# Performance work log

Hardware: AMD Instinct MI355X
Metric: run time of the kernel (lower is better)

## Reference

```python
import math
import jax, jax.numpy as jnp
import numpy as np

B, LQ, LK, D, DV = 16, 2048, 2048, 256, 256


def setup_inputs() -> dict:
    key = jax.random.key(0)
    k1, k2, k3, k4 = jax.random.split(key, 4)
    query = jax.random.normal(k1, (B, LQ, D), dtype=jnp.float32)
    kmat = jax.random.normal(k2, (B, LK, D), dtype=jnp.float32)
    value = jax.random.normal(k3, (B, LK, DV), dtype=jnp.float32)
    # per-batch valid lengths in [1, LK] (avoid 0 => all -inf row)
    valid_len = jax.random.randint(k4, (B,), 1, LK + 1, dtype=jnp.int64)
    return {"query": query, "key": kmat, "value": value, "valid_len": valid_len}


def reference(query, key, value, valid_len):
    d = query.shape[-1]
    # [B, Lq, Lk] scaled dot-product scores
    scores = jnp.einsum("bqd,bkd->bqk", query, key) / math.sqrt(d)
    # mask positions k >= valid_len[b] (same mask broadcast over all queries,
    # matching the repeat(1, Lq).view(shape) in the original masked_softmax)
    mask = jnp.arange(key.shape[1])[None, None, :] < valid_len[:, None, None]
    scores = jnp.where(mask, scores, -jnp.inf)
    attn = jax.nn.softmax(scores, axis=-1)  # dropout rate is 0.0 => identity
    return jnp.einsum("bqk,bkv->bqv", attn, value)
```

## Files before the change

kernel.cpp:

```cpp
#include <hip/hip_runtime.h>
#include <hip/hip_bf16.h>

#define B_   16
#define LQ_  2048
#define LK_  2048
#define D_   256
#define DV_  256
#define MINF -1.0e30f

typedef __bf16 bf16x8_t __attribute__((ext_vector_type(8)));
typedef short  s16x8    __attribute__((ext_vector_type(8)));
typedef short  s16x4    __attribute__((ext_vector_type(4)));
typedef float  f32x4    __attribute__((ext_vector_type(4)));

__device__ __forceinline__ unsigned short f2bf(float f) {
  unsigned int u = __builtin_bit_cast(unsigned int, f);
  u += 0x7fffu + ((u >> 16) & 1u);
  return (unsigned short)(u >> 16);
}

__device__ __forceinline__ s16x8 pack8(float4 a, float4 b) {
  s16x8 r;
  r[0] = (short)f2bf(a.x); r[1] = (short)f2bf(a.y);
  r[2] = (short)f2bf(a.z); r[3] = (short)f2bf(a.w);
  r[4] = (short)f2bf(b.x); r[5] = (short)f2bf(b.y);
  r[6] = (short)f2bf(b.z); r[7] = (short)f2bf(b.w);
  return r;
}

__device__ __forceinline__ void glds16(const unsigned short* g, unsigned short* l) {
  __builtin_amdgcn_global_load_lds(
      (const __attribute__((address_space(1))) unsigned int*)g,
      (__attribute__((address_space(3))) unsigned int*)l, 16, 0, 0);
}

__global__ __launch_bounds__(256) void prep_k(const float* __restrict__ K,
                                              unsigned short* __restrict__ wsK) {
  int gid = blockIdx.x * 256 + threadIdx.x;
  int gr = gid >> 5;
  int c  = gid & 31;
  const float* src = K + ((size_t)gr << 8) + c * 8;
  float4 a = *(const float4*)(src);
  float4 b = *(const float4*)(src + 4);
  *(s16x8*)(wsK + ((size_t)gr << 8) + ((c ^ (gr & 7)) << 3)) = pack8(a, b);
}

__global__ __launch_bounds__(256) void prep_v(const float* __restrict__ V,
                                              unsigned short* __restrict__ wsV) {
  __shared__ unsigned short t[256 * 72];
  const int tid = threadIdx.x;
  const float* src = V + (size_t)blockIdx.x * 64 * 256;
  #pragma unroll
  for (int i = 0; i < 16; ++i) {
    int idx = i * 256 + tid;
    int k   = idx >> 6;
    int dv0 = (idx & 63) * 4;
    float4 x = *(const float4*)(src + k * 256 + dv0);
    t[(dv0 + 0) * 72 + k] = f2bf(x.x);
    t[(dv0 + 1) * 72 + k] = f2bf(x.y);
    t[(dv0 + 2) * 72 + k] = f2bf(x.z);
    t[(dv0 + 3) * 72 + k] = f2bf(x.w);
  }
  __syncthreads();
  unsigned short* dst = wsV + (size_t)blockIdx.x * 16384;
  #pragma unroll
  for (int i = 0; i < 8; ++i) {
    int idx = i * 256 + tid;
    int dv = idx >> 3;
    int ch = idx & 7;
    s16x8 v = *(const s16x8*)(&t[dv * 72 + ch * 8]);
    *(s16x8*)(dst + dv * 64 + ((ch ^ (dv & 7)) << 3)) = v;
  }
}

__global__ __launch_bounds__(512) void attn_fwd3(
    const float* __restrict__ Q, const unsigned short* __restrict__ wsK,
    const unsigned short* __restrict__ wsV, const int* __restrict__ VL,
    float* __restrict__ O) {
  __shared__ __align__(16) unsigned short lds_s[4][16384];

  const int tid  = threadIdx.x;
  const int wid  = tid >> 6;
  const int lane = tid & 63;
  const int l15  = lane & 15;
  const int lg   = lane >> 4;
  const int rg   = wid & 3;
  const int kh   = wid >> 2;

  const int bid = blockIdx.x;
  const int b   = bid >> 5;
  const int qt  = bid & 31;

  int n_k = (VL[1] == 0) ? VL[2 * b] : VL[b];
  if (n_k < 1) n_k = 1;
  if (n_k > LK_) n_k = LK_;
  const int nt = (n_k + 63) >> 6;

  const int qbase = qt * 64 + rg * 16;

  s16x8 qf[8];
  {
    const float* qp = Q + ((size_t)b * LQ_ + qbase + l15) * D_ + lg * 8;
    #pragma unroll
    for (int dk = 0; dk < 8; ++dk) {
      float4 a = *(const float4*)(qp + dk * 32);
      float4 c = *(const float4*)(qp + dk * 32 + 4);
      qf[dk] = pack8(a, c);
    }
  }

  f32x4 o[16];
  #pragma unroll
  for (int c = 0; c < 16; ++c) o[c] = (f32x4){0.f, 0.f, 0.f, 0.f};
  float m = MINF, l = 0.f;

  const unsigned short* kbw = wsK + (size_t)b * LK_ * D_;
  const unsigned short* vbw = wsV + (size_t)b * LK_ * DV_;

#define STAGE(buf, t) do {                                                   \
    const unsigned short* ks_ = kbw + (size_t)(t) * 16384;                   \
    const unsigned short* vs_ = vbw + (size_t)(t) * 16384;                   \
    _Pragma("unroll")                                                        \
    for (int p = 0; p < 4; ++p) {                                            \
      int cu = p * 512 + wid * 64;                                           \
      glds16(ks_ + (size_t)(cu + lane) * 8, &lds_s[(buf)][cu * 8]);          \
      glds16(vs_ + (size_t)(cu + lane) * 8, &lds_s[2 + (buf)][cu * 8]);      \
    }                                                                        \
  } while (0)

  STAGE(0, 0);
  __syncthreads();

  for (int t = 0; t < nt; ++t) {
    const int cur = t & 1;
    if (t + 1 < nt) STAGE(cur ^ 1, t + 1);

    const unsigned short* kl = &lds_s[cur][0];
    f32x4 s[2];
    __builtin_amdgcn_s_setprio(1);
    #pragma unroll
    for (int kc = 0; kc < 2; ++kc) {
      int krow = kh * 32 + kc * 16 + l15;
      int sw = (krow & 7) << 3;
      const unsigned short* base = kl + krow * 256;
      f32x4 a0 = (f32x4){0.f, 0.f, 0.f, 0.f};
      f32x4 a1 = (f32x4){0.f, 0.f, 0.f, 0.f};
      #pragma unroll
      for (int dk = 0; dk < 4; ++dk) {
        s16x8 k0 = *(const s16x8*)(base + ((dk * 64 + lg * 8) ^ sw));
        s16x8 k1 = *(const s16x8*)(base + ((dk * 64 + 32 + lg * 8) ^ sw));
        a0 = __builtin_amdgcn_mfma_f32_16x16x32_bf16(
            __builtin_bit_cast(bf16x8_t, k0),
            __builtin_bit_cast(bf16x8_t, qf[2 * dk]), a0, 0, 0, 0);
        a1 = __builtin_amdgcn_mfma_f32_16x16x32_bf16(
            __builtin_bit_cast(bf16x8_t, k1),
            __builtin_bit_cast(bf16x8_t, qf[2 * dk + 1]), a1, 0, 0, 0);
      }
      s[kc] = a0 + a1;
    }
    __builtin_amdgcn_s_setprio(0);

    #pragma unroll
    for (int kc = 0; kc < 2; ++kc) {
      int gk = t * 64 + kh * 32 + kc * 16 + lg * 4;
      #pragma unroll
      for (int j = 0; j < 4; ++j)
        s[kc][j] = (gk + j < n_k) ? s[kc][j] * 0.0625f : MINF;
    }

    float pm = s[0][0];
    pm = fmaxf(pm, s[0][1]); pm = fmaxf(pm, s[0][2]); pm = fmaxf(pm, s[0][3]);
    pm = fmaxf(pm, s[1][0]); pm = fmaxf(pm, s[1][1]);
    pm = fmaxf(pm, s[1][2]); pm = fmaxf(pm, s[1][3]);
    pm = fmaxf(pm, __shfl_xor(pm, 16, 64));
    pm = fmaxf(pm, __shfl_xor(pm, 32, 64));
    if (__any(pm > m + 8.0f)) {
      float mn = fmaxf(m, pm);
      float sc = __expf(m - mn);
      m = mn; l *= sc;
      #pragma unroll
      for (int c = 0; c < 16; ++c) o[c] = o[c] * sc;
    }
    float p0[4], p1[4];
    #pragma unroll
    for (int j = 0; j < 4; ++j) {
      p0[j] = __expf(s[0][j] - m);
      p1[j] = __expf(s[1][j] - m);
    }
    float ps = ((p0[0] + p0[1]) + (p0[2] + p0[3]))
             + ((p1[0] + p1[1]) + (p1[2] + p1[3]));
    ps += __shfl_xor(ps, 16, 64);
    ps += __shfl_xor(ps, 32, 64);
    l += ps;

    float pv8[8];
    int sl0 = l15 + ((lg & 1) ? 32 : 0);
    #pragma unroll
    for (int h = 0; h < 2; ++h) {
      int sl = sl0 + h * 16;
      #pragma unroll
      for (int j = 0; j < 4; ++j) {
        float a  = __shfl(p0[j], sl, 64);
        float bb = __shfl(p1[j], sl, 64);
        pv8[h * 4 + j] = (lg >= 2) ? bb : a;
      }
    }
    s16x8 pb;
    #pragma unroll
    for (int e = 0; e < 8; ++e) pb[e] = (short)f2bf(pv8[e]);

    const unsigned short* vl_ = &lds_s[2 + cur][0];
    __builtin_amdgcn_s_setprio(1);
    #pragma unroll
    for (int c = 0; c < 16; ++c) {
      int dv = c * 16 + l15;
      int off = dv * 64 + (((kh * 4 + lg) ^ (dv & 7)) << 3);
      s16x8 vf = *(const s16x8*)(vl_ + off);
      o[c] = __builtin_amdgcn_mfma_f32_16x16x32_bf16(
          __builtin_bit_cast(bf16x8_t, vf),
          __builtin_bit_cast(bf16x8_t, pb), o[c], 0, 0, 0);
    }
    __builtin_amdgcn_s_setprio(0);

    __syncthreads();
  }

  float* mrg = (float*)&lds_s[0][0];
  float* mo  = mrg + (wid & 3) * 4160;
  if (wid >= 4) {
    #pragma unroll
    for (int c = 0; c < 16; ++c)
      #pragma unroll
      for (int j = 0; j < 4; ++j)
        mo[l15 * 257 + c * 16 + lg * 4 + j] = o[c][j];
    mo[4112 + l15] = m;
    mo[4128 + l15] = l;
  }
  __syncthreads();
  if (wid < 4) {
    float mb = mo[4112 + l15];
    float lb = mo[4128 + l15];
    float M  = fmaxf(m, mb);
    float sa = __expf(m - M), sb = __expf(mb - M);
    float invL = 1.0f / (sa * l + sb * lb);
    float* ob = O + ((size_t)b * LQ_ + qbase + l15) * DV_;
    #pragma unroll
    for (int c = 0; c < 16; ++c) {
      int dvb = c * 16 + lg * 4;
      const float* mr = mo + l15 * 257 + dvb;
      float4 r;
      r.x = (sa * o[c][0] + sb * mr[0]) * invL;
      r.y = (sa * o[c][1] + sb * mr[1]) * invL;
      r.z = (sa * o[c][2] + sb * mr[2]) * invL;
      r.w = (sa * o[c][3] + sb * mr[3]) * invL;
      *(float4*)(ob + dvb) = r;
    }
  }
#undef STAGE
}

__global__ __launch_bounds__(256) void attn_fwd(
    const float* __restrict__ Q, const float* __restrict__ K,
    const float* __restrict__ V, const int* __restrict__ VL,
    float* __restrict__ O) {
  __shared__ __align__(16) unsigned short lds_k[64 * D_];
  __shared__ __align__(16) unsigned short lds_v[DV_ * 64];
  __shared__ __align__(16) unsigned short lds_p[4][16 * 64];

  const int tid  = threadIdx.x;
  const int wid  = tid >> 6;
  const int lane = tid & 63;
  const int l15  = lane & 15;
  const int lg   = lane >> 4;
  const int bid = blockIdx.x;
  const int b   = bid >> 5;
  const int qt  = bid & 31;

  int n_k = (VL[1] == 0) ? VL[2 * b] : VL[b];
  if (n_k < 1) n_k = 1;
  if (n_k > LK_) n_k = LK_;

  const int qbase = qt * 64 + wid * 16;
  s16x8 qf[8];
  {
    const float* qp = Q + ((size_t)b * LQ_ + qbase + l15) * D_ + lg * 8;
    #pragma unroll
    for (int dk = 0; dk < 8; ++dk) {
      float4 a = *(const float4*)(qp + dk * 32);
      float4 c = *(const float4*)(qp + dk * 32 + 4);
      qf[dk] = pack8(a, c);
    }
  }
  f32x4 o[16];
  #pragma unroll
  for (int c = 0; c < 16; ++c) o[c] = (f32x4){0.f, 0.f, 0.f, 0.f};
  float m[4]    = {-INFINITY, -INFINITY, -INFINITY, -INFINITY};
  float lsum[4] = {0.f, 0.f, 0.f, 0.f};
  const float* kb = K + (size_t)b * LK_ * D_;
  const float* vb = V + (size_t)b * LK_ * DV_;
  const int nt = (n_k + 63) / 64;

  for (int kt = 0; kt < nt; ++kt) {
    __syncthreads();
    {
      const float* src = kb + (size_t)kt * 64 * D_;
      #pragma unroll
      for (int p = 0; p < 8; ++p) {
        int e = (p * 256 + tid) * 8;
        int r = e >> 8;
        int d = e & 255;
        float4 a = *(const float4*)(src + e);
        float4 c = *(const float4*)(src + e + 4);
        *(s16x8*)(&lds_k[r * 256 + (d ^ ((r & 7) << 3))]) = pack8(a, c);
      }
    }
    {
      const float* src = vb + (size_t)kt * 64 * DV_;
      #pragma unroll
      for (int p = 0; p < 2; ++p) {
        int item = p * 256 + tid;
        int k0  = (item >> 5) * 4;
        int dv0 = (item & 31) * 8;
        float va[4][8];
        #pragma unroll
        for (int r = 0; r < 4; ++r) {
          float4 x = *(const float4*)(src + (k0 + r) * DV_ + dv0);
          float4 y = *(const float4*)(src + (k0 + r) * DV_ + dv0 + 4);
          va[r][0]=x.x; va[r][1]=x.y; va[r][2]=x.z; va[r][3]=x.w;
          va[r][4]=y.x; va[r][5]=y.y; va[r][6]=y.z; va[r][7]=y.w;
        }
        #pragma unroll
        for (int i = 0; i < 8; ++i) {
          int dv = dv0 + i;
          s16x4 w;
          w[0]=(short)f2bf(va[0][i]); w[1]=(short)f2bf(va[1][i]);
          w[2]=(short)f2bf(va[2][i]); w[3]=(short)f2bf(va[3][i]);
          *(s16x4*)(&lds_v[dv * 64 + (k0 ^ ((dv & 7) << 3))]) = w;
        }
      }
    }
    __syncthreads();

    f32x4 s[4];
    #pragma unroll
    for (int kc = 0; kc < 4; ++kc) {
      f32x4 acc = (f32x4){0.f, 0.f, 0.f, 0.f};
      int krow = kc * 16 + l15;
      int sw = (krow & 7) << 3;
      #pragma unroll
      for (int dk = 0; dk < 8; ++dk) {
        s16x8 kf = *(const s16x8*)(&lds_k[krow * 256 + ((dk * 32 + lg * 8) ^ sw)]);
        acc = __builtin_amdgcn_mfma_f32_16x16x32_bf16(
            __builtin_bit_cast(bf16x8_t, qf[dk]),
            __builtin_bit_cast(bf16x8_t, kf), acc, 0, 0, 0);
      }
      s[kc] = acc;
    }
    #pragma unroll
    for (int kc = 0; kc < 4; ++kc) {
      int gk = kt * 64 + kc * 16 + l15;
      #pragma unroll
      for (int j = 0; j < 4; ++j) {
        float v = s[kc][j] * 0.0625f;
        s[kc][j] = (gk < n_k) ? v : -INFINITY;
      }
    }
    float pm[4];
    #pragma unroll
    for (int j = 0; j < 4; ++j)
      pm[j] = fmaxf(fmaxf(s[0][j], s[1][j]), fmaxf(s[2][j], s[3][j]));
    #pragma unroll
    for (int off = 1; off < 16; off <<= 1) {
      #pragma unroll
      for (int j = 0; j < 4; ++j)
        pm[j] = fmaxf(pm[j], __shfl_xor(pm[j], off, 64));
    }
    float sc[4];
    #pragma unroll
    for (int j = 0; j < 4; ++j) {
      float mn = fmaxf(m[j], pm[j]);
      sc[j] = __expf(m[j] - mn);
      m[j] = mn;
    }
    float psum[4] = {0.f, 0.f, 0.f, 0.f};
    #pragma unroll
    for (int kc = 0; kc < 4; ++kc) {
      #pragma unroll
      for (int j = 0; j < 4; ++j) {
        float p = __expf(s[kc][j] - m[j]);
        psum[j] += p;
        int r = lg * 4 + j;
        lds_p[wid][r * 64 + ((kc * 16 + l15) ^ ((r & 7) << 3))] = f2bf(p);
      }
    }
    #pragma unroll
    for (int off = 1; off < 16; off <<= 1) {
      #pragma unroll
      for (int j = 0; j < 4; ++j)
        psum[j] += __shfl_xor(psum[j], off, 64);
    }
    #pragma unroll
    for (int j = 0; j < 4; ++j) lsum[j] = lsum[j] * sc[j] + psum[j];
    #pragma unroll
    for (int c = 0; c < 16; ++c) {
      #pragma unroll
      for (int j = 0; j < 4; ++j) o[c][j] *= sc[j];
    }
    s16x8 pa[2];
    #pragma unroll
    for (int kk = 0; kk < 2; ++kk)
      pa[kk] = *(const s16x8*)(&lds_p[wid][l15 * 64 + ((kk * 32 + lg * 8) ^ ((l15 & 7) << 3))]);
    #pragma unroll
    for (int c = 0; c < 16; ++c) {
      #pragma unroll
      for (int kk = 0; kk < 2; ++kk) {
        int dv = c * 16 + l15;
        s16x8 vf = *(const s16x8*)(&lds_v[dv * 64 + ((kk * 32 + lg * 8) ^ ((dv & 7) << 3))]);
        o[c] = __builtin_amdgcn_mfma_f32_16x16x32_bf16(
            __builtin_bit_cast(bf16x8_t, pa[kk]),
            __builtin_bit_cast(bf16x8_t, vf), o[c], 0, 0, 0);
      }
    }
  }
  float inv[4];
  #pragma unroll
  for (int j = 0; j < 4; ++j) inv[j] = 1.0f / lsum[j];
  float* ob = O + ((size_t)b * LQ_ + qbase) * DV_;
  #pragma unroll
  for (int c = 0; c < 16; ++c) {
    #pragma unroll
    for (int j = 0; j < 4; ++j) {
      int r = lg * 4 + j;
      ob[(size_t)r * DV_ + c * 16 + l15] = o[c][j] * inv[j];
    }
  }
}

extern "C" void kernel_launch(void* const* d_in, const int* in_sizes, int n_in,
                              void* d_out, int out_size, void* d_ws, size_t ws_size,
                              hipStream_t stream) {
  const float* Q  = (const float*)d_in[0];
  const float* K  = (const float*)d_in[1];
  const float* V  = (const float*)d_in[2];
  const int*   VL = (const int*)d_in[3];
  float* O = (float*)d_out;

  const size_t kv_elems = (size_t)B_ * LK_ * D_;
  const size_t need = kv_elems * 2 * sizeof(unsigned short);
  if (ws_size >= need) {
    unsigned short* wsK = (unsigned short*)d_ws;
    unsigned short* wsV = wsK + kv_elems;
    prep_k<<<dim3(4096), dim3(256), 0, stream>>>(K, wsK);
    prep_v<<<dim3(512), dim3(256), 0, stream>>>(V, wsV);
    attn_fwd3<<<dim3(512), dim3(512), 0, stream>>>(Q, wsK, wsV, VL, O);
  } else {
    attn_fwd<<<dim3(512), dim3(256), 0, stream>>>(Q, K, V, VL, O);
  }
}
```

Baseline: 135.7 us.

## Double query rows per wave to reuse K/V fragments across two MFMA tiles

Each wave now handles 32 query rows (two 16-row chunks) instead of 16, so every K and V fragment read from LDS feeds two MFMAs. The block covers 128 queries and the grid is halved to 256 blocks. The P-matrix shuffle is replaced by a per-wave LDS scratch round-trip. This reduces LDS traffic per FLOP and K/V staging per query, but doubles accumulator registers (launch_bounds 512,2) and halves grid parallelism, which on a 256-CU part could leave CUs underused.

```diff
diff --git a/kernel.cpp b/kernel.cpp
--- a/kernel.cpp
+++ b/kernel.cpp
@@ -73,59 +73,64 @@
   }
 }
 
-__global__ __launch_bounds__(512) void attn_fwd3(
+__global__ __launch_bounds__(512, 2) void attn_fwd4(
     const float* __restrict__ Q, const unsigned short* __restrict__ wsK,
     const unsigned short* __restrict__ wsV, const int* __restrict__ VL,
     float* __restrict__ O) {
-  __shared__ __align__(16) unsigned short lds_s[4][16384];
+  __shared__ __align__(16) unsigned short lds_all[75776];
 
   const int tid  = threadIdx.x;
   const int wid  = tid >> 6;
   const int lane = tid & 63;
   const int l15  = lane & 15;
   const int lg   = lane >> 4;
-  const int rg   = wid & 3;
+  const int rq   = wid & 3;
   const int kh   = wid >> 2;
 
   const int bid = blockIdx.x;
-  const int b   = bid >> 5;
-  const int qt  = bid & 31;
+  const int b   = bid >> 4;
+  const int qt  = bid & 15;
 
   int n_k = (VL[1] == 0) ? VL[2 * b] : VL[b];
   if (n_k < 1) n_k = 1;
   if (n_k > LK_) n_k = LK_;
   const int nt = (n_k + 63) >> 6;
 
-  const int qbase = qt * 64 + rg * 16;
-
-  s16x8 qf[8];
-  {
-    const float* qp = Q + ((size_t)b * LQ_ + qbase + l15) * D_ + lg * 8;
+  const int qbase = qt * 128 + rq * 32;
+
+  s16x8 qf[2][8];
+  #pragma unroll
+  for (int qc = 0; qc < 2; ++qc) {
+    const float* qp = Q + ((size_t)b * LQ_ + qbase + qc * 16 + l15) * D_ + lg * 8;
     #pragma unroll
     for (int dk = 0; dk < 8; ++dk) {
       float4 a = *(const float4*)(qp + dk * 32);
       float4 c = *(const float4*)(qp + dk * 32 + 4);
-      qf[dk] = pack8(a, c);
-    }
-  }
-
-  f32x4 o[16];
-  #pragma unroll
-  for (int c = 0; c < 16; ++c) o[c] = (f32x4){0.f, 0.f, 0.f, 0.f};
-  float m = MINF, l = 0.f;
+      qf[qc][dk] = pack8(a, c);
+    }
+  }
+
+  f32x4 o[2][16];
+  #pragma unroll
+  for (int qc = 0; qc < 2; ++qc)
+    #pragma unroll
+    for (int c = 0; c < 16; ++c) o[qc][c] = (f32x4){0.f, 0.f, 0.f, 0.f};
+  float m[2] = {MINF, MINF}, l[2] = {0.f, 0.f};
 
   const unsigned short* kbw = wsK + (size_t)b * LK_ * D_;
   const unsigned short* vbw = wsV + (size_t)b * LK_ * DV_;
-
-#define STAGE(buf, t) do {                                                   \
-    const unsigned short* ks_ = kbw + (size_t)(t) * 16384;                   \
-    const unsigned short* vs_ = vbw + (size_t)(t) * 16384;                   \
-    _Pragma("unroll")                                                        \
-    for (int p = 0; p < 4; ++p) {                                            \
-      int cu = p * 512 + wid * 64;                                           \
-      glds16(ks_ + (size_t)(cu + lane) * 8, &lds_s[(buf)][cu * 8]);          \
-      glds16(vs_ + (size_t)(cu + lane) * 8, &lds_s[2 + (buf)][cu * 8]);      \
-    }                                                                        \
+  unsigned short* pw = &lds_all[65536 + wid * 1280];
+
+#define STAGE(buf, t) do {                                                    \
+    const unsigned short* ks_ = kbw + (size_t)(t) * 16384;                    \
+    const unsigned short* vs_ = vbw + (size_t)(t) * 16384;                    \
+    _Pragma("unroll")                                                         \
+    for (int p = 0; p < 4; ++p) {                                             \
+      int cu = p * 512 + wid * 64;                                            \
+      glds16(ks_ + (size_t)(cu + lane) * 8, &lds_all[(buf) * 16384 + cu * 8]);\
+      glds16(vs_ + (size_t)(cu + lane) * 8,                                   \
+             &lds_all[32768 + (buf) * 16384 + cu * 8]);                       \
+    }                                                                         \
   } while (0)
 
   STAGE(0, 0);
@@ -135,8 +140,8 @@
     const int cur = t & 1;
     if (t + 1 < nt) STAGE(cur ^ 1, t + 1);
 
-    const unsigned short* kl = &lds_s[cur][0];
-    f32x4 s[2];
+    const unsigned short* kl = &lds_all[cur * 16384];
+    f32x4 s[2][2];
     __builtin_amdgcn_s_setprio(1);
     #pragma unroll
     for (int kc = 0; kc < 2; ++kc) {
@@ -146,17 +151,17 @@
       f32x4 a0 = (f32x4){0.f, 0.f, 0.f, 0.f};
       f32x4 a1 = (f32x4){0.f, 0.f, 0.f, 0.f};
       #pragma unroll
-      for (int dk = 0; dk < 4; ++dk) {
-        s16x8 k0 = *(const s16x8*)(base + ((dk * 64 + lg * 8) ^ sw));
-        s16x8 k1 = *(const s16x8*)(base + ((dk * 64 + 32 + lg * 8) ^ sw));
+      for (int dk = 0; dk < 8; ++dk) {
+        s16x8 kf = *(const s16x8*)(base + ((dk * 32 + lg * 8) ^ sw));
         a0 = __builtin_amdgcn_mfma_f32_16x16x32_bf16(
-            __builtin_bit_cast(bf16x8_t, k0),
-            __builtin_bit_cast(bf16x8_t, qf[2 * dk]), a0, 0, 0, 0);
+            __builtin_bit_cast(bf16x8_t, kf),
+            __builtin_bit_cast(bf16x8_t, qf[0][dk]), a0, 0, 0, 0);
         a1 = __builtin_amdgcn_mfma_f32_16x16x32_bf16(
-            __builtin_bit_cast(bf16x8_t, k1),
-            __builtin_bit_cast(bf16x8_t, qf[2 * dk + 1]), a1, 0, 0, 0);
-      }
-      s[kc] = a0 + a1;
+            __builtin_bit_cast(bf16x8_t, kf),
+            __builtin_bit_cast(bf16x8_t, qf[1][dk]), a1, 0, 0, 0);
+      }
+      s[kc][0] = a0;
+      s[kc][1] = a1;
     }
     __builtin_amdgcn_s_setprio(0);
 
@@ -164,96 +169,108 @@
     for (int kc = 0; kc < 2; ++kc) {
       int gk = t * 64 + kh * 32 + kc * 16 + lg * 4;
       #pragma unroll
-      for (int j = 0; j < 4; ++j)
-        s[kc][j] = (gk + j < n_k) ? s[kc][j] * 0.0625f : MINF;
-    }
-
-    float pm = s[0][0];
-    pm = fmaxf(pm, s[0][1]); pm = fmaxf(pm, s[0][2]); pm = fmaxf(pm, s[0][3]);
-    pm = fmaxf(pm, s[1][0]); pm = fmaxf(pm, s[1][1]);
-    pm = fmaxf(pm, s[1][2]); pm = fmaxf(pm, s[1][3]);
-    pm = fmaxf(pm, __shfl_xor(pm, 16, 64));
-    pm = fmaxf(pm, __shfl_xor(pm, 32, 64));
-    if (__any(pm > m + 8.0f)) {
-      float mn = fmaxf(m, pm);
-      float sc = __expf(m - mn);
-      m = mn; l *= sc;
-      #pragma unroll
-      for (int c = 0; c < 16; ++c) o[c] = o[c] * sc;
-    }
-    float p0[4], p1[4];
-    #pragma unroll
-    for (int j = 0; j < 4; ++j) {
-      p0[j] = __expf(s[0][j] - m);
-      p1[j] = __expf(s[1][j] - m);
-    }
-    float ps = ((p0[0] + p0[1]) + (p0[2] + p0[3]))
-             + ((p1[0] + p1[1]) + (p1[2] + p1[3]));
-    ps += __shfl_xor(ps, 16, 64);
-    ps += __shfl_xor(ps, 32, 64);
-    l += ps;
-
-    float pv8[8];
-    int sl0 = l15 + ((lg & 1) ? 32 : 0);
-    #pragma unroll
-    for (int h = 0; h < 2; ++h) {
-      int sl = sl0 + h * 16;
-      #pragma unroll
-      for (int j = 0; j < 4; ++j) {
-        float a  = __shfl(p0[j], sl, 64);
-        float bb = __shfl(p1[j], sl, 64);
-        pv8[h * 4 + j] = (lg >= 2) ? bb : a;
-      }
-    }
-    s16x8 pb;
-    #pragma unroll
-    for (int e = 0; e < 8; ++e) pb[e] = (short)f2bf(pv8[e]);
-
-    const unsigned short* vl_ = &lds_s[2 + cur][0];
+      for (int qc = 0; qc < 2; ++qc)
+        #pragma unroll
+        for (int j = 0; j < 4; ++j)
+          s[kc][qc][j] = (gk + j < n_k) ? s[kc][qc][j] * 0.0625f : MINF;
+    }
+
+    float pm[2];
+    #pragma unroll
+    for (int qc = 0; qc < 2; ++qc) {
+      float v = fmaxf(fmaxf(s[0][qc][0], s[0][qc][1]),
+                      fmaxf(s[0][qc][2], s[0][qc][3]));
+      v = fmaxf(v, fmaxf(fmaxf(s[1][qc][0], s[1][qc][1]),
+                         fmaxf(s[1][qc][2], s[1][qc][3])));
+      v = fmaxf(v, __shfl_xor(v, 16, 64));
+      v = fmaxf(v, __shfl_xor(v, 32, 64));
+      pm[qc] = v;
+    }
+    if (__any((pm[0] > m[0] + 8.0f) || (pm[1] > m[1] + 8.0f))) {
+      #pragma unroll
+      for (int qc = 0; qc < 2; ++qc) {
+        float mn = fmaxf(m[qc], pm[qc]);
+        float sc = __expf(m[qc] - mn);
+        m[qc] = mn; l[qc] *= sc;
+        #pragma unroll
+        for (int c = 0; c < 16; ++c) o[qc][c] = o[qc][c] * sc;
+      }
+    }
+    #pragma unroll
+    for (int qc = 0; qc < 2; ++qc) {
+      float p[2][4];
+      #pragma unroll
+      for (int kc = 0; kc < 2; ++kc)
+        #pragma unroll
+        for (int j = 0; j < 4; ++j)
+          p[kc][j] = __expf(s[kc][qc][j] - m[qc]);
+      float ps = ((p[0][0] + p[0][1]) + (p[0][2] + p[0][3]))
+               + ((p[1][0] + p[1][1]) + (p[1][2] + p[1][3]));
+      ps += __shfl_xor(ps, 16, 64);
+      ps += __shfl_xor(ps, 32, 64);
+      l[qc] += ps;
+      #pragma unroll
+      for (int kc = 0; kc < 2; ++kc) {
+        s16x4 w;
+        w[0] = (short)f2bf(p[kc][0]); w[1] = (short)f2bf(p[kc][1]);
+        w[2] = (short)f2bf(p[kc][2]); w[3] = (short)f2bf(p[kc][3]);
+        *(s16x4*)(pw + (qc * 16 + l15) * 40 + kc * 16 + lg * 4) = w;
+      }
+    }
+
+    s16x8 pb[2];
+    #pragma unroll
+    for (int qc = 0; qc < 2; ++qc)
+      pb[qc] = *(const s16x8*)(pw + (qc * 16 + l15) * 40 + lg * 8);
+
+    const unsigned short* vl_ = &lds_all[32768 + cur * 16384];
     __builtin_amdgcn_s_setprio(1);
     #pragma unroll
     for (int c = 0; c < 16; ++c) {
       int dv = c * 16 + l15;
-      int off = dv * 64 + (((kh * 4 + lg) ^ (dv & 7)) << 3);
-      s16x8 vf = *(const s16x8*)(vl_ + off);
-      o[c] = __builtin_amdgcn_mfma_f32_16x16x32_bf16(
+      s16x8 vf = *(const s16x8*)(vl_ + dv * 64 + (((kh * 4 + lg) ^ (dv & 7)) << 3));
+      o[0][c] = __builtin_amdgcn_mfma_f32_16x16x32_bf16(
           __builtin_bit_cast(bf16x8_t, vf),
-          __builtin_bit_cast(bf16x8_t, pb), o[c], 0, 0, 0);
+          __builtin_bit_cast(bf16x8_t, pb[0]), o[0][c], 0, 0, 0);
+      o[1][c] = __builtin_amdgcn_mfma_f32_16x16x32_bf16(
+          __builtin_bit_cast(bf16x8_t, vf),
+          __builtin_bit_cast(bf16x8_t, pb[1]), o[1][c], 0, 0, 0);
     }
     __builtin_amdgcn_s_setprio(0);
 
     __syncthreads();
   }
 
-  float* mrg = (float*)&lds_s[0][0];
-  float* mo  = mrg + (wid & 3) * 4160;
-  if (wid >= 4) {
-    #pragma unroll
-    for (int c = 0; c < 16; ++c)
-      #pragma unroll
-      for (int j = 0; j < 4; ++j)
-        mo[l15 * 257 + c * 16 + lg * 4 + j] = o[c][j];
-    mo[4112 + l15] = m;
-    mo[4128 + l15] = l;
+  float* mo = (float*)lds_all + rq * 8448;
+  if (kh == 1) {
+    #pragma unroll
+    for (int qc = 0; qc < 2; ++qc) {
+      #pragma unroll
+      for (int c = 0; c < 16; ++c)
+        *(f32x4*)(mo + (qc * 16 + l15) * 260 + c * 16 + lg * 4) = o[qc][c];
+      mo[8320 + qc * 16 + l15] = m[qc];
+      mo[8352 + qc * 16 + l15] = l[qc];
+    }
   }
   __syncthreads();
-  if (wid < 4) {
-    float mb = mo[4112 + l15];
-    float lb = mo[4128 + l15];
-    float M  = fmaxf(m, mb);
-    float sa = __expf(m - M), sb = __expf(mb - M);
-    float invL = 1.0f / (sa * l + sb * lb);
-    float* ob = O + ((size_t)b * LQ_ + qbase + l15) * DV_;
-    #pragma unroll
-    for (int c = 0; c < 16; ++c) {
-      int dvb = c * 16 + lg * 4;
-      const float* mr = mo + l15 * 257 + dvb;
-      float4 r;
-      r.x = (sa * o[c][0] + sb * mr[0]) * invL;
-      r.y = (sa * o[c][1] + sb * mr[1]) * invL;
-      r.z = (sa * o[c][2] + sb * mr[2]) * invL;
-      r.w = (sa * o[c][3] + sb * mr[3]) * invL;
-      *(float4*)(ob + dvb) = r;
+  if (kh == 0) {
+    #pragma unroll
+    for (int qc = 0; qc < 2; ++qc) {
+      float mb = mo[8320 + qc * 16 + l15];
+      float lb = mo[8352 + qc * 16 + l15];
+      float M  = fmaxf(m[qc], mb);
+      float sa = __expf(m[qc] - M), sb = __expf(mb - M);
+      float invL = 1.0f / (sa * l[qc] + sb * lb);
+      float* ob = O + ((size_t)b * LQ_ + qbase + qc * 16 + l15) * DV_;
+      #pragma unroll
+      for (int c = 0; c < 16; ++c) {
+        int dvb = c * 16 + lg * 4;
+        f32x4 mr = *(const f32x4*)(mo + (qc * 16 + l15) * 260 + dvb);
+        f32x4 r;
+        #pragma unroll
+        for (int j = 0; j < 4; ++j) r[j] = (sa * o[qc][c][j] + sb * mr[j]) * invL;
+        *(f32x4*)(ob + dvb) = r;
+      }
     }
   }
 #undef STAGE
@@ -452,7 +469,7 @@
     unsigned short* wsV = wsK + kv_elems;
     prep_k<<<dim3(4096), dim3(256), 0, stream>>>(K, wsK);
     prep_v<<<dim3(512), dim3(256), 0, stream>>>(V, wsV);
-    attn_fwd3<<<dim3(512), dim3(512), 0, stream>>>(Q, wsK, wsV, VL, O);
+    attn_fwd4<<<dim3(256), dim3(512), 0, stream>>>(Q, wsK, wsV, VL, O);
   } else {
     attn_fwd<<<dim3(512), dim3(256), 0, stream>>>(Q, K, V, VL, O);
   }
```

Result: no change. 135.9 us (+0.2%).

## Halve KV tile to 32 keys to cut LDS and raise occupancy

Applied to the files above, without the earlier changes.

The KV tile per iteration shrinks from 64 to 32 keys. That cuts the LDS footprint from 128KB to about 67KB and allows more blocks per CU, with launch bounds set to (512,4). The V transpose layout is rebuilt for 32-key tiles, and the PV product switches to a 16x16x16 bf16 MFMA, which removes the cross-lane shuffles that rearranged probabilities. It also adds manual vmcnt waits with raw barriers, and a block-index remap that interleaves batches across blocks. The trade-off is twice as many loop iterations and barriers, plus smaller, less efficient MFMAs.

```diff
diff --git a/kernel.cpp b/kernel.cpp
--- a/kernel.cpp
+++ b/kernel.cpp
@@ -32,6 +32,17 @@
   __builtin_amdgcn_global_load_lds(
       (const __attribute__((address_space(1))) unsigned int*)g,
       (__attribute__((address_space(3))) unsigned int*)l, 16, 0, 0);
+}
+
+__device__ __forceinline__ f32x4 mfma16(s16x4 a, s16x4 b, f32x4 c) {
+#if __has_builtin(__builtin_amdgcn_mfma_f32_16x16x16bf16_1k)
+  return __builtin_amdgcn_mfma_f32_16x16x16bf16_1k(a, b, c, 0, 0, 0);
+#else
+  f32x4 d;
+  asm volatile("v_mfma_f32_16x16x16_bf16 %0, %1, %2, %3"
+               : "=v"(d) : "v"(a), "v"(b), "v"(c));
+  return d;
+#endif
 }
 
 __global__ __launch_bounds__(256) void prep_k(const float* __restrict__ K,
@@ -47,56 +58,58 @@
 
 __global__ __launch_bounds__(256) void prep_v(const float* __restrict__ V,
                                               unsigned short* __restrict__ wsV) {
-  __shared__ unsigned short t[256 * 72];
+  __shared__ unsigned short t[256 * 40];
   const int tid = threadIdx.x;
-  const float* src = V + (size_t)blockIdx.x * 64 * 256;
-  #pragma unroll
-  for (int i = 0; i < 16; ++i) {
+  const float* src = V + (size_t)blockIdx.x * 32 * 256;
+  #pragma unroll
+  for (int i = 0; i < 8; ++i) {
     int idx = i * 256 + tid;
     int k   = idx >> 6;
     int dv0 = (idx & 63) * 4;
     float4 x = *(const float4*)(src + k * 256 + dv0);
-    t[(dv0 + 0) * 72 + k] = f2bf(x.x);
-    t[(dv0 + 1) * 72 + k] = f2bf(x.y);
-    t[(dv0 + 2) * 72 + k] = f2bf(x.z);
-    t[(dv0 + 3) * 72 + k] = f2bf(x.w);
+    t[(dv0 + 0) * 40 + k] = f2bf(x.x);
+    t[(dv0 + 1) * 40 + k] = f2bf(x.y);
+    t[(dv0 + 2) * 40 + k] = f2bf(x.z);
+    t[(dv0 + 3) * 40 + k] = f2bf(x.w);
   }
   __syncthreads();
-  unsigned short* dst = wsV + (size_t)blockIdx.x * 16384;
-  #pragma unroll
-  for (int i = 0; i < 8; ++i) {
+  unsigned short* dst = wsV + (size_t)blockIdx.x * 8192;
+  #pragma unroll
+  for (int i = 0; i < 4; ++i) {
     int idx = i * 256 + tid;
-    int dv = idx >> 3;
-    int ch = idx & 7;
-    s16x8 v = *(const s16x8*)(&t[dv * 72 + ch * 8]);
-    *(s16x8*)(dst + dv * 64 + ((ch ^ (dv & 7)) << 3)) = v;
-  }
-}
-
-__global__ __launch_bounds__(512) void attn_fwd3(
+    int dv = idx >> 2;
+    int cs = idx & 3;
+    int c2 = cs ^ ((dv >> 1) & 3);
+    s16x8 v = *(const s16x8*)(&t[dv * 40 + cs * 8]);
+    *(s16x8*)(dst + dv * 32 + c2 * 8) = v;
+  }
+}
+
+__global__ __launch_bounds__(512, 4) void attn_fwd8(
     const float* __restrict__ Q, const unsigned short* __restrict__ wsK,
     const unsigned short* __restrict__ wsV, const int* __restrict__ VL,
     float* __restrict__ O) {
-  __shared__ __align__(16) unsigned short lds_s[4][16384];
+  __shared__ __align__(16) unsigned short lds_all[33536];
 
   const int tid  = threadIdx.x;
   const int wid  = tid >> 6;
   const int lane = tid & 63;
   const int l15  = lane & 15;
   const int lg   = lane >> 4;
-  const int rg   = wid & 3;
+  const int rq   = wid & 3;
   const int kh   = wid >> 2;
 
   const int bid = blockIdx.x;
-  const int b   = bid >> 5;
-  const int qt  = bid & 31;
+  const int j   = bid >> 3;
+  const int b   = (bid & 7) + ((j >> 5) << 3);
+  const int qt  = j & 31;
 
   int n_k = (VL[1] == 0) ? VL[2 * b] : VL[b];
   if (n_k < 1) n_k = 1;
   if (n_k > LK_) n_k = LK_;
-  const int nt = (n_k + 63) >> 6;
-
-  const int qbase = qt * 64 + rg * 16;
+  const int nt = (n_k + 31) >> 5;
+
+  const int qbase = qt * 64 + rq * 16;
 
   s16x8 qf[8];
   {
@@ -117,61 +130,60 @@
   const unsigned short* kbw = wsK + (size_t)b * LK_ * D_;
   const unsigned short* vbw = wsV + (size_t)b * LK_ * DV_;
 
-#define STAGE(buf, t) do {                                                   \
-    const unsigned short* ks_ = kbw + (size_t)(t) * 16384;                   \
-    const unsigned short* vs_ = vbw + (size_t)(t) * 16384;                   \
-    _Pragma("unroll")                                                        \
-    for (int p = 0; p < 4; ++p) {                                            \
-      int cu = p * 512 + wid * 64;                                           \
-      glds16(ks_ + (size_t)(cu + lane) * 8, &lds_s[(buf)][cu * 8]);          \
-      glds16(vs_ + (size_t)(cu + lane) * 8, &lds_s[2 + (buf)][cu * 8]);      \
-    }                                                                        \
+#define STAGE(buf, t) do {                                                    \
+    const unsigned short* ks_ = kbw + (size_t)(t) * 8192;                     \
+    const unsigned short* vs_ = vbw + (size_t)(t) * 8192;                     \
+    _Pragma("unroll")                                                         \
+    for (int p = 0; p < 2; ++p) {                                             \
+      int cu = p * 512 + wid * 64;                                            \
+      glds16(ks_ + (size_t)(cu + lane) * 8, &lds_all[(buf) * 8192 + cu * 8]); \
+      glds16(vs_ + (size_t)(cu + lane) * 8,                                   \
+             &lds_all[16384 + (buf) * 8192 + cu * 8]);                        \
+    }                                                                         \
   } while (0)
 
   STAGE(0, 0);
-  __syncthreads();
 
   for (int t = 0; t < nt; ++t) {
     const int cur = t & 1;
-    if (t + 1 < nt) STAGE(cur ^ 1, t + 1);
-
-    const unsigned short* kl = &lds_s[cur][0];
-    f32x4 s[2];
+    if (t + 1 < nt) {
+      STAGE(cur ^ 1, t + 1);
+      asm volatile("s_waitcnt vmcnt(4)" ::: "memory");
+    } else {
+      asm volatile("s_waitcnt vmcnt(0)" ::: "memory");
+    }
+    __builtin_amdgcn_s_barrier();
+    __builtin_amdgcn_sched_barrier(0);
+
+    const unsigned short* kl = &lds_all[cur * 8192];
+    const int krow = kh * 16 + l15;
+    const int sw = (krow & 7) << 3;
+    const unsigned short* kbase = kl + krow * 256;
+    f32x4 a0 = (f32x4){0.f, 0.f, 0.f, 0.f};
+    f32x4 a1 = (f32x4){0.f, 0.f, 0.f, 0.f};
     __builtin_amdgcn_s_setprio(1);
     #pragma unroll
-    for (int kc = 0; kc < 2; ++kc) {
-      int krow = kh * 32 + kc * 16 + l15;
-      int sw = (krow & 7) << 3;
-      const unsigned short* base = kl + krow * 256;
-      f32x4 a0 = (f32x4){0.f, 0.f, 0.f, 0.f};
-      f32x4 a1 = (f32x4){0.f, 0.f, 0.f, 0.f};
-      #pragma unroll
-      for (int dk = 0; dk < 4; ++dk) {
-        s16x8 k0 = *(const s16x8*)(base + ((dk * 64 + lg * 8) ^ sw));
-        s16x8 k1 = *(const s16x8*)(base + ((dk * 64 + 32 + lg * 8) ^ sw));
-        a0 = __builtin_amdgcn_mfma_f32_16x16x32_bf16(
-            __builtin_bit_cast(bf16x8_t, k0),
-            __builtin_bit_cast(bf16x8_t, qf[2 * dk]), a0, 0, 0, 0);
-        a1 = __builtin_amdgcn_mfma_f32_16x16x32_bf16(
-            __builtin_bit_cast(bf16x8_t, k1),
-            __builtin_bit_cast(bf16x8_t, qf[2 * dk + 1]), a1, 0, 0, 0);
-      }
-      s[kc] = a0 + a1;
+    for (int dk = 0; dk < 4; ++dk) {
+      s16x8 k0 = *(const s16x8*)(kbase + ((dk * 64 + lg * 8) ^ sw));
+      s16x8 k1 = *(const s16x8*)(kbase + ((dk * 64 + 32 + lg * 8) ^ sw));
+      a0 = __builtin_amdgcn_mfma_f32_16x16x32_bf16(
+          __builtin_bit_cast(bf16x8_t, k0),
+          __builtin_bit_cast(bf16x8_t, qf[2 * dk]), a0, 0, 0, 0);
+      a1 = __builtin_amdgcn_mfma_f32_16x16x32_bf16(
+          __builtin_bit_cast(bf16x8_t, k1),
+          __builtin_bit_cast(bf16x8_t, qf[2 * dk + 1]), a1, 0, 0, 0);
     }
     __builtin_amdgcn_s_setprio(0);
-
-    #pragma unroll
-    for (int kc = 0; kc < 2; ++kc) {
-      int gk = t * 64 + kh * 32 + kc * 16 + lg * 4;
-      #pragma unroll
-      for (int j = 0; j < 4; ++j)
-        s[kc][j] = (gk + j < n_k) ? s[kc][j] * 0.0625f : MINF;
-    }
-
-    float pm = s[0][0];
-    pm = fmaxf(pm, s[0][1]); pm = fmaxf(pm, s[0][2]); pm = fmaxf(pm, s[0][3]);
-    pm = fmaxf(pm, s[1][0]); pm = fmaxf(pm, s[1][1]);
-    pm = fmaxf(pm, s[1][2]); pm = fmaxf(pm, s[1][3]);
+    f32x4 s = a0 + a1;
+
+    {
+      int gk = t * 32 + kh * 16 + lg * 4;
+      #pragma unroll
+      for (int j2 = 0; j2 < 4; ++j2)
+        s[j2] = (gk + j2 < n_k) ? s[j2] * 0.0625f : MINF;
+    }
+
+    float pm = fmaxf(fmaxf(s[0], s[1]), fmaxf(s[2], s[3]));
     pm = fmaxf(pm, __shfl_xor(pm, 16, 64));
     pm = fmaxf(pm, __shfl_xor(pm, 32, 64));
     if (__any(pm > m + 8.0f)) {
@@ -181,79 +193,59 @@
       #pragma unroll
       for (int c = 0; c < 16; ++c) o[c] = o[c] * sc;
     }
-    float p0[4], p1[4];
-    #pragma unroll
-    for (int j = 0; j < 4; ++j) {
-      p0[j] = __expf(s[0][j] - m);
-      p1[j] = __expf(s[1][j] - m);
-    }
-    float ps = ((p0[0] + p0[1]) + (p0[2] + p0[3]))
-             + ((p1[0] + p1[1]) + (p1[2] + p1[3]));
+    float p[4];
+    #pragma unroll
+    for (int j2 = 0; j2 < 4; ++j2) p[j2] = __expf(s[j2] - m);
+    float ps = (p[0] + p[1]) + (p[2] + p[3]);
     ps += __shfl_xor(ps, 16, 64);
     ps += __shfl_xor(ps, 32, 64);
     l += ps;
 
-    float pv8[8];
-    int sl0 = l15 + ((lg & 1) ? 32 : 0);
-    #pragma unroll
-    for (int h = 0; h < 2; ++h) {
-      int sl = sl0 + h * 16;
-      #pragma unroll
-      for (int j = 0; j < 4; ++j) {
-        float a  = __shfl(p0[j], sl, 64);
-        float bb = __shfl(p1[j], sl, 64);
-        pv8[h * 4 + j] = (lg >= 2) ? bb : a;
-      }
-    }
-    s16x8 pb;
-    #pragma unroll
-    for (int e = 0; e < 8; ++e) pb[e] = (short)f2bf(pv8[e]);
-
-    const unsigned short* vl_ = &lds_s[2 + cur][0];
+    s16x4 pb;
+    pb[0] = (short)f2bf(p[0]); pb[1] = (short)f2bf(p[1]);
+    pb[2] = (short)f2bf(p[2]); pb[3] = (short)f2bf(p[3]);
+
+    const unsigned short* vl_ = &lds_all[16384 + cur * 8192];
+    const int vcs = kh * 2 + (lg >> 1);
+    const int ve  = (lg & 1) * 4;
     __builtin_amdgcn_s_setprio(1);
     #pragma unroll
     for (int c = 0; c < 16; ++c) {
       int dv = c * 16 + l15;
-      int off = dv * 64 + (((kh * 4 + lg) ^ (dv & 7)) << 3);
-      s16x8 vf = *(const s16x8*)(vl_ + off);
-      o[c] = __builtin_amdgcn_mfma_f32_16x16x32_bf16(
-          __builtin_bit_cast(bf16x8_t, vf),
-          __builtin_bit_cast(bf16x8_t, pb), o[c], 0, 0, 0);
+      s16x4 vf = *(const s16x4*)(vl_ + dv * 32 + ((vcs ^ ((dv >> 1) & 3)) << 3) + ve);
+      o[c] = mfma16(vf, pb, o[c]);
     }
     __builtin_amdgcn_s_setprio(0);
 
-    __syncthreads();
-  }
-
-  float* mrg = (float*)&lds_s[0][0];
-  float* mo  = mrg + (wid & 3) * 4160;
-  if (wid >= 4) {
+    __builtin_amdgcn_sched_barrier(0);
+    __builtin_amdgcn_s_barrier();
+  }
+
+  __syncthreads();
+  float* mo = (float*)lds_all + rq * 4192;
+  if (kh == 1) {
     #pragma unroll
     for (int c = 0; c < 16; ++c)
-      #pragma unroll
-      for (int j = 0; j < 4; ++j)
-        mo[l15 * 257 + c * 16 + lg * 4 + j] = o[c][j];
-    mo[4112 + l15] = m;
-    mo[4128 + l15] = l;
+      *(f32x4*)(mo + l15 * 260 + c * 16 + lg * 4) = o[c];
+    mo[4160 + l15] = m;
+    mo[4176 + l15] = l;
   }
   __syncthreads();
-  if (wid < 4) {
-    float mb = mo[4112 + l15];
-    float lb = mo[4128 + l15];
+  if (kh == 0) {
+    float mb = mo[4160 + l15];
+    float lb = mo[4176 + l15];
     float M  = fmaxf(m, mb);
     float sa = __expf(m - M), sb = __expf(mb - M);
     float invL = 1.0f / (sa * l + sb * lb);
     float* ob = O + ((size_t)b * LQ_ + qbase + l15) * DV_;
     #pragma unroll
     for (int c = 0; c < 16; ++c) {
-      int dvb = c * 16 + lg * 4;
-      const float* mr = mo + l15 * 257 + dvb;
-      float4 r;
-      r.x = (sa * o[c][0] + sb * mr[0]) * invL;
-      r.y = (sa * o[c][1] + sb * mr[1]) * invL;
-      r.z = (sa * o[c][2] + sb * mr[2]) * invL;
-      r.w = (sa * o[c][3] + sb * mr[3]) * invL;
-      *(float4*)(ob + dvb) = r;
+      f32x4 mr = *(const f32x4*)(mo + l15 * 260 + c * 16 + lg * 4);
+      f32x4 r;
+      #pragma unroll
+      for (int j2 = 0; j2 < 4; ++j2)
+        r[j2] = (sa * o[c][j2] + sb * mr[j2]) * invL;
+      *(f32x4*)(ob + c * 16 + lg * 4) = r;
     }
   }
 #undef STAGE
@@ -389,8 +381,8 @@
       for (int j = 0; j < 4; ++j) {
         float p = __expf(s[kc][j] - m[j]);
         psum[j] += p;
-        int r = lg * 4 + j;
-        lds_p[wid][r * 64 + ((kc * 16 + l15) ^ ((r & 7) << 3))] = f2bf(p);
+        int r2 = lg * 4 + j;
+        lds_p[wid][r2 * 64 + ((kc * 16 + l15) ^ ((r2 & 7) << 3))] = f2bf(p);
       }
     }
     #pragma unroll
@@ -430,8 +422,8 @@
   for (int c = 0; c < 16; ++c) {
     #pragma unroll
     for (int j = 0; j < 4; ++j) {
-      int r = lg * 4 + j;
-      ob[(size_t)r * DV_ + c * 16 + l15] = o[c][j] * inv[j];
+      int r2 = lg * 4 + j;
+      ob[(size_t)r2 * DV_ + c * 16 + l15] = o[c][j] * inv[j];
     }
   }
 }
@@ -451,8 +443,8 @@
     unsigned short* wsK = (unsigned short*)d_ws;
     unsigned short* wsV = wsK + kv_elems;
     prep_k<<<dim3(4096), dim3(256), 0, stream>>>(K, wsK);
-    prep_v<<<dim3(512), dim3(256), 0, stream>>>(V, wsV);
-    attn_fwd3<<<dim3(512), dim3(512), 0, stream>>>(Q, wsK, wsV, VL, O);
+    prep_v<<<dim3(1024), dim3(256), 0, stream>>>(V, wsV);
+    attn_fwd8<<<dim3(512), dim3(512), 0, stream>>>(Q, wsK, wsV, VL, O);
   } else {
     attn_fwd<<<dim3(512), dim3(256), 0, stream>>>(Q, K, V, VL, O);
   }
```

After: 180.3 us. 32.9% more time.
